# Performance work log

Measured on AMD Instinct MI355X. Metric: run time of the kernel, lower is better.

Reference implementation:

```python
import jax, jax.numpy as jnp
import numpy as np

B, N, D, H, EF = 8, 1024, 768, 8, 4
S = D * EF          # sparse_dim = 3072
HD = S // H         # head_dim = 384
HUB_POW = 1.5
PERSIST = 0.95
EPS = 1e-6
LN_EPS = 1e-5


def setup_inputs() -> dict:
    key = jax.random.key(0)
    ks = jax.random.split(key, 8)
    s = 0.02  # weight init scale
    return {
        "x": jax.random.normal(ks[0], (B, N, D), jnp.float32),
        "memory": jax.random.normal(ks[1], (H, HD, HD), jnp.float32) * 0.01,
        "ln_g": jnp.ones((D,), jnp.float32),
        "ln_b": jnp.zeros((D,), jnp.float32),
        "w_in": jax.random.normal(ks[2], (D, 3 * S), jnp.float32) * s,
        "b_in": jnp.zeros((3 * S,), jnp.float32),
        "w_out": jax.random.normal(ks[3], (S, D), jnp.float32) * s,
        "b_out": jnp.zeros((D,), jnp.float32),
        "w_rg": jax.random.normal(ks[4], (D, H), jnp.float32) * s,
        "b_rg": jnp.zeros((H,), jnp.float32),
        "w_wg": jax.random.normal(ks[5], (D, H), jnp.float32) * s,
        "b_wg": jnp.zeros((H,), jnp.float32),
        "w_res": jax.random.normal(ks[6], (D, 1), jnp.float32) * s,
        "b_res": jnp.zeros((1,), jnp.float32),
    }


def reference(x, memory, ln_g, ln_b, w_in, b_in, w_out, b_out,
              w_rg, b_rg, w_wg, b_wg, w_res, b_res):
    residual = x
    # LayerNorm (biased variance, matching torch)
    mu = x.mean(axis=-1, keepdims=True)
    var = x.var(axis=-1, keepdims=True)
    xn = (x - mu) / jnp.sqrt(var + LN_EPS) * ln_g + ln_b

    qkv = xn @ w_in + b_in                      # [B,N,3S]
    q, k, v = jnp.split(qkv, 3, axis=-1)

    def to_heads(t):                            # [B,N,S] -> [B,H,N,hd]
        return t.reshape(B, N, H, HD).transpose(0, 2, 1, 3)

    # power-law hub feature map
    q = jnp.power(jax.nn.relu(to_heads(q)) + EPS, HUB_POW)
    k = jnp.power(jax.nn.relu(to_heads(k)) + EPS, HUB_POW)
    v = to_heads(v)
    # normalize k over the token axis
    k = k / (k.sum(axis=2, keepdims=True) + EPS)

    # per-head linear-attention state: k^T @ v -> [B,H,hd,hd]
    batch_state = jnp.einsum('bhnd,bhne->bhde', k, v)

    x_mean = xn.mean(axis=1)                    # [B,D]
    read = jax.nn.sigmoid(x_mean @ w_rg + b_rg)[:, :, None, None]   # [B,H,1,1]
    write = jax.nn.sigmoid(x_mean @ w_wg + b_wg)[:, :, None, None]  # [B,H,1,1]
    residue = jax.nn.sigmoid(xn @ w_res + b_res)                    # [B,N,1]

    # gated EMA memory update (update happens BEFORE read, as in source)
    state_mean = batch_state.mean(axis=0)       # [H,hd,hd]
    mem_new = PERSIST * memory + (1.0 - PERSIST) * write.mean(axis=0) * state_mean

    # read from updated persistent memory
    y = jnp.einsum('bhnd,bhde->bhne', q, mem_new[None] * read)
    y = y.transpose(0, 2, 1, 3).reshape(B, N, S)

    out = residue * (y @ w_out + b_out) + (1.0 - residue) * residual
    return out
```

## Files before the change

kernel.cpp:

```cpp
#include <hip/hip_runtime.h>
#include <hip/hip_bf16.h>
#include <cstdint>
#include <cstddef>


typedef __bf16 bf16_t;
typedef bf16_t bf16x4 __attribute__((ext_vector_type(4)));
typedef bf16_t bf16x8 __attribute__((ext_vector_type(8)));
typedef float f32x4 __attribute__((ext_vector_type(4)));

#define AS1 __attribute__((address_space(1)))
#define AS3 __attribute__((address_space(3)))

__device__ __forceinline__ void gemm128_bt(
    const bf16_t* __restrict__ A, int lda,
    const bf16_t* __restrict__ BT, int ldb,
    int K, int row0, int col0,
    bf16_t* As, bf16_t* Bs, f32x4 acc[4][4])
{
    const int t    = threadIdx.x;
    const int lane = t & 63;
    const int wid  = t >> 6;
    const int wr   = wid >> 1, wc = wid & 1;
    const int fr   = lane & 15;
    const int fk   = (lane >> 4) * 8;

#pragma unroll
    for (int m = 0; m < 4; ++m)
#pragma unroll
        for (int n = 0; n < 4; ++n)
            acc[m][n] = (f32x4){0.f, 0.f, 0.f, 0.f};

    const int rr = lane >> 2;
    const int rc = (lane & 3) * 8;

    for (int k0 = 0; k0 < K; k0 += 32) {
#pragma unroll
        for (int c = 0; c < 2; ++c) {
            const int q = wid * 2 + c;
            __builtin_amdgcn_global_load_lds(
                (const AS1 void*)(A + (size_t)(row0 + q * 16 + rr) * lda + (k0 + rc)),
                (AS3 void*)(As + q * 512), 16, 0, 0);
            __builtin_amdgcn_global_load_lds(
                (const AS1 void*)(BT + (size_t)(col0 + q * 16 + rr) * ldb + (k0 + rc)),
                (AS3 void*)(Bs + q * 512), 16, 0, 0);
        }
        __syncthreads();

        bf16x8 av[4], bv[4];
#pragma unroll
        for (int m = 0; m < 4; ++m)
            av[m] = *(const bf16x8*)&As[(wr * 64 + m * 16 + fr) * 32 + fk];
#pragma unroll
        for (int n = 0; n < 4; ++n)
            bv[n] = *(const bf16x8*)&Bs[(wc * 64 + n * 16 + fr) * 32 + fk];
#pragma unroll
        for (int m = 0; m < 4; ++m)
#pragma unroll
            for (int n = 0; n < 4; ++n)
                acc[m][n] = __builtin_amdgcn_mfma_f32_16x16x32_bf16(av[m], bv[n], acc[m][n], 0, 0, 0);
        __syncthreads();
    }
}

__device__ __forceinline__ void band_map(int flat, int nby, int& bx, int& by)
{
    const int xcd = flat & 7;
    const int seq = flat >> 3;
    const int bandsz = nby >> 3;
    by = xcd * bandsz + (seq % bandsz);
    bx = seq / bandsz;
}


__global__ void ktrans_w(const float* __restrict__ in, bf16_t* __restrict__ out, int R, int C)
{
    __shared__ float tl[32][33];
    const int c0 = blockIdx.x * 32, r0 = blockIdx.y * 32;
    const int tx = threadIdx.x, ty = threadIdx.y;
#pragma unroll
    for (int i = ty; i < 32; i += 8) tl[i][tx] = in[(size_t)(r0 + i) * C + c0 + tx];
    __syncthreads();
#pragma unroll
    for (int i = ty; i < 32; i += 8) out[(size_t)(c0 + i) * R + r0 + tx] = (bf16_t)tl[tx][i];
}

__device__ __forceinline__ float block_sum256(float v, float* s4)
{
#pragma unroll
    for (int off = 32; off > 0; off >>= 1) v += __shfl_down(v, off);
    const int lane = threadIdx.x & 63, w = threadIdx.x >> 6;
    if (lane == 0) s4[w] = v;
    __syncthreads();
    return s4[0] + s4[1] + s4[2] + s4[3];
}

__global__ void __launch_bounds__(256) kln(
    const float* __restrict__ x, const float* __restrict__ g, const float* __restrict__ bt,
    const float* __restrict__ w_res, const float* __restrict__ b_res,
    bf16_t* __restrict__ xn, float* __restrict__ residue)
{
    __shared__ float red[12];
    const int row = blockIdx.x;
    const float* xr = x + (size_t)row * 768;
    const int t = threadIdx.x;
    const float v0 = xr[t], v1 = xr[t + 256], v2 = xr[t + 512];
    const float ts  = block_sum256(v0 + v1 + v2, red);
    const float ts2 = block_sum256(v0 * v0 + v1 * v1 + v2 * v2, red + 4);
    const float mu  = ts * (1.f / 768.f);
    const float var = ts2 * (1.f / 768.f) - mu * mu;
    const float rs  = rsqrtf(var + 1e-5f);
    float dot = 0.f;
    {
        float xv;
        xv = (v0 - mu) * rs * g[t]       + bt[t];       xn[(size_t)row * 768 + t]       = (bf16_t)xv; dot += xv * w_res[t];
        xv = (v1 - mu) * rs * g[t + 256] + bt[t + 256]; xn[(size_t)row * 768 + t + 256] = (bf16_t)xv; dot += xv * w_res[t + 256];
        xv = (v2 - mu) * rs * g[t + 512] + bt[t + 512]; xn[(size_t)row * 768 + t + 512] = (bf16_t)xv; dot += xv * w_res[t + 512];
    }
    const float td = block_sum256(dot, red + 8);
    if (t == 0) residue[row] = 1.f / (1.f + expf(-(td + b_res[0])));
}

__global__ void kcolmean(const bf16_t* __restrict__ xn, float* __restrict__ xmean)
{
    const int b = blockIdx.x, dc = blockIdx.y, nc = blockIdx.z;
    const int d = dc * 256 + threadIdx.x;
    const bf16_t* p = xn + (size_t)(b * 1024 + nc * 128) * 768 + d;
    float s = 0.f;
#pragma unroll 4
    for (int n = 0; n < 128; ++n) s += (float)p[(size_t)n * 768];
    atomicAdd(&xmean[b * 768 + d], s);
}

__global__ void __launch_bounds__(256) kgates(
    const float* __restrict__ xmean,
    const float* __restrict__ w_rg, const float* __restrict__ b_rg,
    const float* __restrict__ w_wg, const float* __restrict__ b_wg,
    float* __restrict__ read_g, float* __restrict__ wmean)
{
    __shared__ float pr[64][4], pw[64][4], wg[64];
    const int t = threadIdx.x, grp = t >> 2, qtr = t & 3;
    const int b = grp >> 3, h = grp & 7;
    float dr = 0.f, dw = 0.f;
    for (int d = qtr * 192; d < qtr * 192 + 192; ++d) {
        const float xm = xmean[b * 768 + d] * (1.f / 1024.f);
        dr += xm * w_rg[d * 8 + h];
        dw += xm * w_wg[d * 8 + h];
    }
    pr[grp][qtr] = dr; pw[grp][qtr] = dw;
    __syncthreads();
    if (qtr == 0) {
        const float sr = pr[grp][0] + pr[grp][1] + pr[grp][2] + pr[grp][3];
        const float sw = pw[grp][0] + pw[grp][1] + pw[grp][2] + pw[grp][3];
        read_g[grp] = 1.f / (1.f + expf(-(sr + b_rg[h])));
        wg[grp]     = 1.f / (1.f + expf(-(sw + b_wg[h])));
    }
    __syncthreads();
    if (t < 8) {
        float s = 0.f;
#pragma unroll
        for (int b2 = 0; b2 < 8; ++b2) s += wg[b2 * 8 + t];
        wmean[t] = s * 0.125f;
    }
}

__global__ void __launch_bounds__(512) kgemm_qkv256(
    const bf16_t* __restrict__ xnc, const bf16_t* __restrict__ w_inT,
    const float* __restrict__ b_in, const float* __restrict__ rg_c,
    bf16_t* __restrict__ qfc, bf16_t* __restrict__ kTc, bf16_t* __restrict__ vTc,
    float* __restrict__ ksum_c, int nrt )
{
    __shared__ __align__(16) bf16_t L[65536];
    const int t = threadIdx.x, lane = t & 63, wid = t >> 6;
    const int wr = wid >> 2, wc = wid & 3;
    int bx, by;
    band_map(blockIdx.y * 36 + blockIdx.x, nrt, bx, by);
    const int row0 = by * 256, col0 = bx * 256;

    f32x4 acc[8][4];
#pragma unroll
    for (int m = 0; m < 8; ++m)
#pragma unroll
        for (int n = 0; n < 4; ++n)
            acc[m][n] = (f32x4){0.f, 0.f, 0.f, 0.f};

    const int sgrow = wid * 16 + (lane >> 2);
    const int sgcol = (((lane & 3) ^ ((lane >> 3) & 3)) * 8);
    const int xslot = (((lane >> 4) ^ ((lane >> 1) & 3))) * 8;
    const int fr = lane & 15;

    auto stage = [&](int buf, int k0) {
        bf16_t* base = &L[buf * 16384];
#pragma unroll
        for (int op = 0; op < 2; ++op) {
            const bf16_t* src = op ? w_inT : xnc;
            const int r0 = op ? col0 : row0;
#pragma unroll
            for (int i = 0; i < 2; ++i)
                __builtin_amdgcn_global_load_lds(
                    (const AS1 void*)(src + (size_t)(r0 + i * 128 + sgrow) * 768 + (k0 + sgcol)),
                    (AS3 void*)(base + op * 8192 + i * 4096 + wid * 512), 16, 0, 0);
        }
    };

    bf16x8 avA[8], bvA[4], avB[8], bvB[4];
    auto ldfrags = [&](int buf, bf16x8 (&av)[8], bf16x8 (&bv)[4]) {
        const bf16_t* base = &L[buf * 16384];
#pragma unroll
        for (int n = 0; n < 4; ++n)
            bv[n] = *(const bf16x8*)&base[8192 + (wc * 64 + n * 16 + fr) * 32 + xslot];
#pragma unroll
        for (int m = 0; m < 8; ++m)
            av[m] = *(const bf16x8*)&base[(wr * 128 + m * 16 + fr) * 32 + xslot];
    };

    stage(0, 0); stage(1, 32); stage(2, 64); stage(3, 96);
    asm volatile("s_waitcnt vmcnt(12)" ::: "memory");
    __builtin_amdgcn_s_barrier();
    __builtin_amdgcn_sched_barrier(0);
    ldfrags(0, avA, bvA);
    asm volatile("s_waitcnt lgkmcnt(0)" ::: "memory");

    const int NT = 24;
    auto body = [&](int ti, bf16x8 (&avc)[8], bf16x8 (&bvc)[4],
                            bf16x8 (&avn)[8], bf16x8 (&bvn)[4]) {
        if (ti < NT - 1) {
            if (ti <= 20)      asm volatile("s_waitcnt vmcnt(8)" ::: "memory");
            else if (ti == 21) asm volatile("s_waitcnt vmcnt(4)" ::: "memory");
            else               asm volatile("s_waitcnt vmcnt(0)" ::: "memory");
            __builtin_amdgcn_s_barrier();
            __builtin_amdgcn_sched_barrier(0);
            ldfrags((ti + 1) & 3, avn, bvn);
            if (ti + 4 < NT) stage(ti & 3, (ti + 4) * 32);
        }
        __builtin_amdgcn_s_setprio(1);
#pragma unroll
        for (int m = 0; m < 8; ++m)
#pragma unroll
            for (int n = 0; n < 4; ++n)
                acc[m][n] = __builtin_amdgcn_mfma_f32_16x16x32_bf16(avc[m], bvc[n], acc[m][n], 0, 0, 0);
        __builtin_amdgcn_s_setprio(0);
        if (ti < NT - 1) asm volatile("s_waitcnt lgkmcnt(0)" ::: "memory");
    };

    for (int tt = 0; tt < NT; tt += 2) {
        body(tt,     avA, bvA, avB, bvB);
        body(tt + 1, avB, bvB, avA, bvA);
    }

    const int third = col0 / 3072;
    const int lb = row0 >> 10;
    if (third == 0) {
#pragma unroll
        for (int n2 = 0; n2 < 4; ++n2) {
            const int col  = col0 + wc * 64 + n2 * 16 + fr;
            const int h    = col / 384;
            const float rg = rg_c[lb * 8 + h];
            const float bias = b_in[col];
#pragma unroll
            for (int m = 0; m < 8; ++m) {
#pragma unroll
                for (int r = 0; r < 4; ++r) {
                    const int row = row0 + wr * 128 + m * 16 + (lane >> 4) * 4 + r;
                    const float v = acc[m][n2][r] + bias;
                    const float u = fmaxf(v, 0.f) + 1e-6f;
                    qfc[(size_t)row * 3072 + col] = (bf16_t)(rg * u * sqrtf(u));
                }
            }
        }
    } else {
        const int nbb = (row0 & 1023) + wr * 128 + (lane >> 4) * 4;
#pragma unroll
        for (int n2 = 0; n2 < 4; ++n2) {
            const int colg = col0 + wc * 64 + n2 * 16 + fr;
            const int coll = colg - third * 3072;
            const int h = coll / 384, d = coll % 384;
            bf16_t* dstT = ((third == 1) ? kTc : vTc) + (size_t)(lb * 8 + h) * 393216;
            const float bias = b_in[colg];
            float ksp = 0.f;
#pragma unroll
            for (int m = 0; m < 8; ++m) {
                bf16x4 pk;
#pragma unroll
                for (int r = 0; r < 4; ++r) {
                    float v = acc[m][n2][r] + bias;
                    if (third == 1) { const float u = fmaxf(v, 0.f) + 1e-6f; v = u * sqrtf(u); ksp += v; }
                    pk[r] = (bf16_t)v;
                }
                *(bf16x4*)&dstT[(size_t)d * 1024 + nbb + m * 16] = pk;
            }
            if (third == 1) atomicAdd(&ksum_c[(size_t)(lb * 8 + h) * 384 + d], ksp);
        }
    }
}

__global__ void __launch_bounds__(256) kgemm_state(
    const bf16_t* __restrict__ kTc, const bf16_t* __restrict__ vTc,
    const float* __restrict__ ksum_c, float* __restrict__ ssum)
{
    __shared__ __align__(16) bf16_t As[4096], Bs[4096];
    const int lbh = blockIdx.z, h = lbh & 7;
    const int row0 = blockIdx.y * 128, col0 = blockIdx.x * 128;
    const bf16_t* A  = kTc + (size_t)lbh * 393216;
    const bf16_t* BT = vTc + (size_t)lbh * 393216;
    f32x4 acc[4][4];
    gemm128_bt(A, 1024, BT, 1024, 1024, row0, col0, As, Bs, acc);

    const int lane = threadIdx.x & 63, wid = threadIdx.x >> 6;
    const int wr = wid >> 1, wc = wid & 1;
    float* ss = ssum + (size_t)h * 147456;
#pragma unroll
    for (int m = 0; m < 4; ++m) {
#pragma unroll
        for (int r = 0; r < 4; ++r) {
            const int d = row0 + wr * 64 + m * 16 + (lane >> 4) * 4 + r;
            const float sc = 1.f / (ksum_c[(size_t)lbh * 384 + d] + 1e-6f);
#pragma unroll
            for (int n = 0; n < 4; ++n) {
                const int e = col0 + wc * 64 + n * 16 + (lane & 15);
                atomicAdd(&ss[(size_t)d * 384 + e], acc[m][n][r] * sc);
            }
        }
    }
}

__global__ void kmemupd_ew(const float* __restrict__ mem, const float* __restrict__ ssum,
                           const float* __restrict__ wmean, bf16_t* __restrict__ mem_new)
{
    const int idx = blockIdx.x * 256 + threadIdx.x;
    const int h = idx / 147456;
    const float wm = wmean[h] * (0.05f / 8.f);
    mem_new[idx] = (bf16_t)(0.95f * mem[idx] + wm * ssum[idx]);
}

__global__ void __launch_bounds__(256) kgemm_G(
    const bf16_t* __restrict__ w_outT, const bf16_t* __restrict__ mem_new,
    bf16_t* __restrict__ GT)
{
    __shared__ __align__(16) bf16_t As[4096], Bs[4096];
    const int h = blockIdx.z;
    const int row0 = blockIdx.y * 128, col0 = blockIdx.x * 128;
    f32x4 acc[4][4];
    gemm128_bt(w_outT + h * 384, 3072, mem_new + (size_t)h * 147456, 384,
               384, row0, col0, As, Bs, acc);

    const int lane = threadIdx.x & 63, wid = threadIdx.x >> 6;
    const int wr = wid >> 1, wc = wid & 1;
#pragma unroll
    for (int m = 0; m < 4; ++m) {
#pragma unroll
        for (int n = 0; n < 4; ++n) {
            const int d = col0 + wc * 64 + n * 16 + (lane & 15);
#pragma unroll
            for (int r = 0; r < 4; ++r) {
                const int c = row0 + wr * 64 + m * 16 + (lane >> 4) * 4 + r;
                GT[(size_t)c * 3072 + h * 384 + d] = (bf16_t)acc[m][n][r];
            }
        }
    }
}

__global__ void __launch_bounds__(256) kgemm_out(
    const bf16_t* __restrict__ qf, const bf16_t* __restrict__ GT,
    const float* __restrict__ b_out, const float* __restrict__ residue,
    const float* __restrict__ x, float* __restrict__ out)
{
    __shared__ __align__(16) bf16_t As[4096], Bs[4096];
    int bx, by;
    band_map(blockIdx.y * 6 + blockIdx.x, 64, bx, by);
    const int row0 = by * 128, col0 = bx * 128;
    f32x4 acc[4][4];
    gemm128_bt(qf, 3072, GT, 3072, 3072, row0, col0, As, Bs, acc);

    const int lane = threadIdx.x & 63, wid = threadIdx.x >> 6;
    const int wr = wid >> 1, wc = wid & 1;
#pragma unroll
    for (int m = 0; m < 4; ++m) {
#pragma unroll
        for (int n = 0; n < 4; ++n) {
            const int col = col0 + wc * 64 + n * 16 + (lane & 15);
            const float bias = b_out[col];
#pragma unroll
            for (int r = 0; r < 4; ++r) {
                const int row = row0 + wr * 64 + m * 16 + (lane >> 4) * 4 + r;
                const float v = acc[m][n][r] + bias;
                const float rr = residue[row];
                out[(size_t)row * 768 + col] = rr * v + (1.f - rr) * x[(size_t)row * 768 + col];
            }
        }
    }
}

extern "C" void kernel_launch(void* const* d_in, const int* in_sizes, int n_in,
                              void* d_out, int out_size, void* d_ws, size_t ws_size,
                              hipStream_t stream)
{
    (void)in_sizes; (void)n_in; (void)out_size;
    const float* x     = (const float*)d_in[0];
    const float* mem   = (const float*)d_in[1];
    const float* ln_g  = (const float*)d_in[2];
    const float* ln_b  = (const float*)d_in[3];
    const float* w_in  = (const float*)d_in[4];
    const float* b_in  = (const float*)d_in[5];
    const float* w_out = (const float*)d_in[6];
    const float* b_out = (const float*)d_in[7];
    const float* w_rg  = (const float*)d_in[8];
    const float* b_rg  = (const float*)d_in[9];
    const float* w_wg  = (const float*)d_in[10];
    const float* b_wg  = (const float*)d_in[11];
    const float* w_res = (const float*)d_in[12];
    const float* b_res = (const float*)d_in[13];
    float* out = (float*)d_out;

    auto total_for = [&](int c) -> size_t {
        size_t o = 0;
        auto a = [&](size_t b) { o += (b + 255) & ~(size_t)255; };
        a(50331648);
        a(14155776); a(12582912);
        a((size_t)c * 6291456);
        a((size_t)c * 6291456);
        a(4718592); a(4718592); a(2359296);
        a(32768); a(24576); a(98304); a(256); a(256);
        return o;
    };
    int CHUNK = 0;
    for (int c = 8; c >= 2; c >>= 1) if (total_for(c) <= ws_size) { CHUNK = c; break; }
    if (CHUNK == 0) return;

    char* ws = (char*)d_ws;
    size_t off = 0;
    auto alloc = [&](size_t bytes) -> char* {
        char* p = ws + off; off += (bytes + 255) & ~(size_t)255; return p;
    };
    bf16_t* qf      = (bf16_t*)alloc(50331648);
    bf16_t* w_inT   = (bf16_t*)alloc(14155776);
    bf16_t* GT      = w_inT;
    bf16_t* xn      = (bf16_t*)alloc(12582912);
    bf16_t* kTc     = (bf16_t*)alloc((size_t)CHUNK * 6291456);
    bf16_t* vTc     = (bf16_t*)alloc((size_t)CHUNK * 6291456);
    bf16_t* w_outT  = (bf16_t*)alloc(4718592);
    float*  ssum    = (float*) alloc(4718592);
    bf16_t* mem_new = (bf16_t*)alloc(2359296);
    float*  residue = (float*) alloc(32768);
    float*  xmean   = (float*) alloc(24576);
    float*  ksum    = (float*) alloc(98304);
    float*  read_g  = (float*) alloc(256);
    float*  wmean   = (float*) alloc(256);

    hipMemsetAsync(xmean, 0, 24576, stream);
    hipMemsetAsync(ksum,  0, 98304, stream);
    hipMemsetAsync(ssum,  0, 4718592, stream);

    ktrans_w<<<dim3(288, 24), dim3(32, 8), 0, stream>>>(w_in, w_inT, 768, 9216);
    ktrans_w<<<dim3(24, 96), dim3(32, 8), 0, stream>>>(w_out, w_outT, 3072, 768);
    kln<<<8192, 256, 0, stream>>>(x, ln_g, ln_b, w_res, b_res, xn, residue);
    kcolmean<<<dim3(8, 3, 8), 256, 0, stream>>>(xn, xmean);
    kgates<<<1, 256, 0, stream>>>(xmean, w_rg, b_rg, w_wg, b_wg, read_g, wmean);

    const int NC = 8 / CHUNK;
    for (int c = 0; c < NC; ++c) {
        const int b0 = c * CHUNK;
        kgemm_qkv256<<<dim3(36, CHUNK * 4), 512, 0, stream>>>(
            xn + (size_t)b0 * 1024 * 768, w_inT, b_in, read_g + b0 * 8,
            qf + (size_t)b0 * 1024 * 3072, kTc, vTc,
            ksum + (size_t)b0 * 8 * 384, CHUNK * 4);
        kgemm_state<<<dim3(3, 3, CHUNK * 8), 256, 0, stream>>>(
            kTc, vTc, ksum + (size_t)b0 * 8 * 384, ssum);
    }

    kmemupd_ew<<<4608, 256, 0, stream>>>(mem, ssum, wmean, mem_new);
    kgemm_G<<<dim3(3, 6, 8), 256, 0, stream>>>(w_outT, mem_new, GT);
    kgemm_out<<<dim3(6, 64), 256, 0, stream>>>(qf, GT, b_out, residue, x, out);
}
```

Before: 372.5 us.

## Restructure QKV GEMM main loop into half-tile phases for two blocks per CU

Rewrites the QKV GEMM K-loop to split each k-tile into two phases: load half the A fragments, run the MFMAs, then load the other half. The global-to-LDS staging is split per operand across the phases, and register double-buffering of fragments is dropped. Together with launch_bounds(512,2), this cuts register pressure so two 512-thread blocks can share a CU, aiming to overlap memory and compute across blocks. In exchange it adds an extra barrier per tile, removes in-block fragment prefetch, and changes the staging order (the clamped out-of-range prefetch tile is loaded redundantly).

```diff
diff --git a/kernel.cpp b/kernel.cpp
--- a/kernel.cpp
+++ b/kernel.cpp
@@ -164,7 +164,7 @@
     }
 }
 
-__global__ void __launch_bounds__(512) kgemm_qkv256(
+__global__ void __launch_bounds__(512, 2) kgemm_qkv256(
     const bf16_t* __restrict__ xnc, const bf16_t* __restrict__ w_inT,
     const float* __restrict__ b_in, const float* __restrict__ rg_c,
     bf16_t* __restrict__ qfc, bf16_t* __restrict__ kTc, bf16_t* __restrict__ vTc,
@@ -184,68 +184,73 @@
         for (int n = 0; n < 4; ++n)
             acc[m][n] = (f32x4){0.f, 0.f, 0.f, 0.f};
 
-    const int sgrow = wid * 16 + (lane >> 2);
-    const int sgcol = (((lane & 3) ^ ((lane >> 3) & 3)) * 8);
+    const int sgrow = t >> 2;
+    const int sgcol = (((t & 3) ^ ((t >> 3) & 3)) * 8);
     const int xslot = (((lane >> 4) ^ ((lane >> 1) & 3))) * 8;
     const int fr = lane & 15;
 
-    auto stage = [&](int buf, int k0) {
-        bf16_t* base = &L[buf * 16384];
-#pragma unroll
-        for (int op = 0; op < 2; ++op) {
-            const bf16_t* src = op ? w_inT : xnc;
-            const int r0 = op ? col0 : row0;
-#pragma unroll
-            for (int i = 0; i < 2; ++i)
-                __builtin_amdgcn_global_load_lds(
-                    (const AS1 void*)(src + (size_t)(r0 + i * 128 + sgrow) * 768 + (k0 + sgcol)),
-                    (AS3 void*)(base + op * 8192 + i * 4096 + wid * 512), 16, 0, 0);
-        }
+    auto stage2 = [&](int jp, int op) {
+        const int jc = jp > 23 ? 23 : jp;
+        const int k0 = (jc >> 1) * 64 + (jc & 1) * 32;
+        const bf16_t* src = op ? w_inT : xnc;
+        const int r0 = op ? col0 : row0;
+        bf16_t* dst = &L[(jp & 3) * 16384 + op * 8192 + wid * 512];
+#pragma unroll
+        for (int i = 0; i < 2; ++i)
+            __builtin_amdgcn_global_load_lds(
+                (const AS1 void*)(src + (size_t)(r0 + i * 128 + sgrow) * 768 + k0 + sgcol),
+                (AS3 void*)(dst + i * 4096), 16, 0, 0);
     };
 
-    bf16x8 avA[8], bvA[4], avB[8], bvB[4];
-    auto ldfrags = [&](int buf, bf16x8 (&av)[8], bf16x8 (&bv)[4]) {
-        const bf16_t* base = &L[buf * 16384];
+    stage2(0, 0); stage2(0, 1);
+    stage2(1, 0); stage2(1, 1);
+    stage2(2, 0); stage2(2, 1);
+    asm volatile("s_waitcnt vmcnt(8)" ::: "memory");
+    __builtin_amdgcn_s_barrier();
+    __builtin_amdgcn_sched_barrier(0);
+
+    for (int j = 0; j < 24; ++j) {
+        const bf16_t* base = &L[(j & 3) * 16384];
+        bf16x8 av[4], bv[4];
+
 #pragma unroll
         for (int n = 0; n < 4; ++n)
             bv[n] = *(const bf16x8*)&base[8192 + (wc * 64 + n * 16 + fr) * 32 + xslot];
 #pragma unroll
-        for (int m = 0; m < 8; ++m)
+        for (int m = 0; m < 4; ++m)
             av[m] = *(const bf16x8*)&base[(wr * 128 + m * 16 + fr) * 32 + xslot];
-    };
-
-    stage(0, 0); stage(1, 32); stage(2, 64); stage(3, 96);
-    asm volatile("s_waitcnt vmcnt(12)" ::: "memory");
-    __builtin_amdgcn_s_barrier();
-    __builtin_amdgcn_sched_barrier(0);
-    ldfrags(0, avA, bvA);
-    asm volatile("s_waitcnt lgkmcnt(0)" ::: "memory");
-
-    const int NT = 24;
-    auto body = [&](int ti, bf16x8 (&avc)[8], bf16x8 (&bvc)[4],
-                            bf16x8 (&avn)[8], bf16x8 (&bvn)[4]) {
-        if (ti < NT - 1) {
-            if (ti <= 20)      asm volatile("s_waitcnt vmcnt(8)" ::: "memory");
-            else if (ti == 21) asm volatile("s_waitcnt vmcnt(4)" ::: "memory");
-            else               asm volatile("s_waitcnt vmcnt(0)" ::: "memory");
-            __builtin_amdgcn_s_barrier();
-            __builtin_amdgcn_sched_barrier(0);
-            ldfrags((ti + 1) & 3, avn, bvn);
-            if (ti + 4 < NT) stage(ti & 3, (ti + 4) * 32);
-        }
+        stage2(j + 3, 0);
+        asm volatile("s_waitcnt lgkmcnt(0)" ::: "memory");
+        __builtin_amdgcn_sched_barrier(0);
         __builtin_amdgcn_s_setprio(1);
 #pragma unroll
-        for (int m = 0; m < 8; ++m)
+        for (int m = 0; m < 4; ++m)
 #pragma unroll
             for (int n = 0; n < 4; ++n)
-                acc[m][n] = __builtin_amdgcn_mfma_f32_16x16x32_bf16(avc[m], bvc[n], acc[m][n], 0, 0, 0);
+                acc[m][n] = __builtin_amdgcn_mfma_f32_16x16x32_bf16(av[m], bv[n], acc[m][n], 0, 0, 0);
         __builtin_amdgcn_s_setprio(0);
-        if (ti < NT - 1) asm volatile("s_waitcnt lgkmcnt(0)" ::: "memory");
-    };
-
-    for (int tt = 0; tt < NT; tt += 2) {
-        body(tt,     avA, bvA, avB, bvB);
-        body(tt + 1, avB, bvB, avA, bvA);
+        __builtin_amdgcn_sched_barrier(0);
+        __builtin_amdgcn_s_barrier();
+        __builtin_amdgcn_sched_barrier(0);
+
+#pragma unroll
+        for (int m = 0; m < 4; ++m)
+            av[m] = *(const bf16x8*)&base[(wr * 128 + (m + 4) * 16 + fr) * 32 + xslot];
+        stage2(j + 3, 1);
+        asm volatile("s_waitcnt lgkmcnt(0)" ::: "memory");
+        __builtin_amdgcn_sched_barrier(0);
+        __builtin_amdgcn_s_setprio(1);
+#pragma unroll
+        for (int m = 0; m < 4; ++m)
+#pragma unroll
+            for (int n = 0; n < 4; ++n)
+                acc[m + 4][n] = __builtin_amdgcn_mfma_f32_16x16x32_bf16(av[m], bv[n], acc[m + 4][n], 0, 0, 0);
+        __builtin_amdgcn_s_setprio(0);
+        if (j < 23)
+            asm volatile("s_waitcnt vmcnt(8)" ::: "memory");
+        __builtin_amdgcn_sched_barrier(0);
+        __builtin_amdgcn_s_barrier();
+        __builtin_amdgcn_sched_barrier(0);
     }
 
     const int third = col0 / 3072;
```

Measured after the change: 376.7 us. About the same (+1.1%).
